# Kernel tuning notes

Hardware: AMD Instinct MI355X
Metric: run time of the kernel (lower is better)

Reference implementation:

```python
import jax, jax.numpy as jnp
import numpy as np

K = 20
NEG_SLOPE = 0.2
BN_EPS = 1e-5


def _knn_idx(x, k):
    # x: (B, N, C) -> indices of k nearest neighbors (B, N, k) (self included)
    sq = jnp.sum(x * x, axis=-1)                      # (B, N)
    d = sq[:, :, None] - 2.0 * jnp.einsum('bnc,bmc->bnm', x, x) + sq[:, None, :]
    return jax.lax.top_k(-d, k)[1]                    # smallest distances


def _bn_lrelu(y, bn):
    g, b, m, v = bn[0], bn[1], bn[2], bn[3]
    y = (y - m) * (g * jax.lax.rsqrt(v + BN_EPS)) + b
    return jnp.where(y > 0, y, NEG_SLOPE * y)


def _edge_conv(x, W, bn, k):
    # x: (B, N, C); W: (O, 2C); returns (B, N, O)
    idx = _knn_idx(x, k)                              # (B, N, k)
    grouped = jnp.take_along_axis(x[:, None, :, :], idx[..., None], axis=2)  # (B, N, k, C)
    center = x[:, :, None, :]
    edge = jnp.concatenate([grouped - center,
                            jnp.broadcast_to(center, grouped.shape)], axis=-1)  # (B, N, k, 2C)
    y = jnp.einsum('bnkc,oc->bnko', edge, W)          # 1x1 conv, no bias
    y = _bn_lrelu(y, bn)
    return jnp.max(y, axis=2)                         # max over neighbors


def setup_inputs() -> dict:
    key = jax.random.key(0)
    ks = jax.random.split(key, 12)
    B, N = 8, 2048
    x = jax.random.normal(ks[0], (B, N, 3), dtype=jnp.float32)

    def w(k_, o, i):
        return jax.random.normal(k_, (o, i), dtype=jnp.float32) * (1.0 / np.sqrt(i))

    def bn(k_, c):
        k1, k2, k3, k4 = jax.random.split(k_, 4)
        gamma = jax.random.uniform(k1, (c,), jnp.float32) + 0.5
        beta = jax.random.normal(k2, (c,), jnp.float32) * 0.1
        mean = jax.random.normal(k3, (c,), jnp.float32) * 0.1
        var = jax.random.uniform(k4, (c,), jnp.float32) + 0.5
        return jnp.stack([gamma, beta, mean, var])    # (4, C)

    return {
        'x': x,
        'W1': w(ks[1], 64, 6),
        'W2': w(ks[2], 64, 128),
        'W3': w(ks[3], 128, 128),
        'W4': w(ks[4], 256, 256),
        'W5': w(ks[5], 1024, 512),
        'bn1': bn(ks[6], 64),
        'bn2': bn(ks[7], 64),
        'bn3': bn(ks[8], 128),
        'bn4': bn(ks[9], 256),
        'bn5': bn(ks[10], 1024),
    }


def reference(x, W1, W2, W3, W4, W5, bn1, bn2, bn3, bn4, bn5):
    x1 = _edge_conv(x, W1, bn1, K)                    # (B, N, 64)
    x2 = _edge_conv(x1, W2, bn2, K)                   # (B, N, 64)
    x3 = _edge_conv(x2, W3, bn3, K)                   # (B, N, 128)
    x4 = _edge_conv(x3, W4, bn4, K)                   # (B, N, 256)
    x_cat = jnp.concatenate([x1, x2, x3, x4], axis=-1)  # (B, N, 512)
    feat = _bn_lrelu(jnp.einsum('bnc,oc->bno', x_cat, W5), bn5)  # (B, N, 1024)
    g_max = jnp.max(feat, axis=1)
    g_avg = jnp.mean(feat, axis=1)
    return jnp.concatenate([g_max, g_avg], axis=-1)   # (B, 2048)
```

## Files before the change

kernel.cpp:

```cpp
#include <hip/hip_runtime.h>
#include <hip/hip_bf16.h>
#include <math.h>

#define KNN 20
constexpr int NPTS = 2048;
constexpr int NBAT = 8;
constexpr int M_TOT = NBAT * NPTS;

__global__ __launch_bounds__(256) void sqnorm_kernel(const float* __restrict__ X, int lda, int C,
                                                     float* __restrict__ sq) {
  int i = blockIdx.x * 256 + threadIdx.x;
  if (i >= M_TOT) return;
  const float* p = X + (size_t)i * lda;
  float s = 0.f;
  for (int c = 0; c < C; ++c) { float v = p[c]; s = fmaf(v, v, s); }
  sq[i] = s;
}

#define INSERT_CAND(key_, j_)                                  \
  if ((key_) < dl[KNN - 1]) {                                  \
    float _k = (key_); int _j = (j_);                          \
    _Pragma("unroll")                                          \
    for (int p = 0; p < KNN; ++p) {                            \
      bool sw = _k < dl[p];                                    \
      float od = dl[p]; int oi = il[p];                        \
      dl[p] = sw ? _k : od; il[p] = sw ? _j : oi;              \
      _k = sw ? od : _k; _j = sw ? oi : _j;                    \
    }                                                          \
  }

template <int C, int CSPLIT>
__global__ __launch_bounds__(256, 8) void knn5_kernel(const float* __restrict__ X, int lda,
                                                      const float* __restrict__ sq,
                                                      float* __restrict__ pd,
                                                      int* __restrict__ pi) {
  constexpr int ROWS = 32, CHK = 64, KB = 32, SEL = 8;
  constexpr int KP = KB + 4;
  constexpr int DP = CHK + 1;
  constexpr int NKB = (C == 3) ? 1 : C / KB;
  constexpr int XI_W = (C == 3) ? 4 : KP;
  constexpr int SMF = ROWS * XI_W + CHK * XI_W + ROWS * DP;
  __shared__ __align__(16) float smem[SMF];
  float* xi = smem;
  float* xj = smem + ROWS * XI_W;
  float* dist = smem + (ROWS + CHK) * XI_W;

  const int b = blockIdx.z;
  const int m0 = blockIdx.x * ROWS;
  const int jsplit = blockIdx.y * (NPTS / CSPLIT);
  const int t = threadIdx.x;
  const int tx = t & 15, ty = t >> 4;
  const int sr = t >> 3, ss = t & 7;
  const float* Xb = X + (size_t)b * NPTS * lda;
  const float* sqb = sq + b * NPTS;

  float dl[KNN]; int il[KNN];
#pragma unroll
  for (int p = 0; p < KNN; ++p) { dl[p] = INFINITY; il[p] = 0x7fffffff; }

  for (int c0 = 0; c0 < NPTS / CSPLIT; c0 += CHK) {
    const int jb = jsplit + c0;
    float acc[2][4] = {};

    if constexpr (C == 3) {
      __syncthreads();
      for (int e = t; e < ROWS * 3; e += 256) {
        int rr = e / 3, cc = e % 3;
        xi[rr * 4 + cc] = Xb[(size_t)(m0 + rr) * lda + cc];
      }
      for (int e = t; e < CHK * 3; e += 256) {
        int rr = e / 3, cc = e % 3;
        xj[rr * 4 + cc] = Xb[(size_t)(jb + rr) * lda + cc];
      }
      __syncthreads();
#pragma unroll
      for (int i = 0; i < 2; ++i) {
        const float* xr = xi + (ty + 16 * i) * 4;
        float x0 = xr[0], x1 = xr[1], x2 = xr[2];
#pragma unroll
        for (int j = 0; j < 4; ++j) {
          const float* xc = xj + (tx + 16 * j) * 4;
          acc[i][j] = fmaf(x0, xc[0], fmaf(x1, xc[1], x2 * xc[2]));
        }
      }
    } else {
#pragma unroll
      for (int kb = 0; kb < NKB; ++kb) {
        __syncthreads();
#pragma unroll
        for (int q = 0; q < 3; ++q) {
          if (q == 0) {
            int rr = t >> 3, cc = t & 7;
            *(float4*)(xi + rr * KP + cc * 4) =
                *(const float4*)(Xb + (size_t)(m0 + rr) * lda + kb * KB + cc * 4);
          } else {
            int f = t + (q - 1) * 256;
            int rr = f >> 3, cc = f & 7;
            *(float4*)(xj + rr * KP + cc * 4) =
                *(const float4*)(Xb + (size_t)(jb + rr) * lda + kb * KB + cc * 4);
          }
        }
        __syncthreads();
#pragma unroll
        for (int k4 = 0; k4 < KB / 4; ++k4) {
          float4 av[2], bv[4];
#pragma unroll
          for (int i = 0; i < 2; ++i) av[i] = *(const float4*)(xi + (ty + 16 * i) * KP + k4 * 4);
#pragma unroll
          for (int j = 0; j < 4; ++j) bv[j] = *(const float4*)(xj + (tx + 16 * j) * KP + k4 * 4);
#pragma unroll
          for (int i = 0; i < 2; ++i)
#pragma unroll
            for (int j = 0; j < 4; ++j) {
              acc[i][j] = fmaf(av[i].x, bv[j].x, acc[i][j]);
              acc[i][j] = fmaf(av[i].y, bv[j].y, acc[i][j]);
              acc[i][j] = fmaf(av[i].z, bv[j].z, acc[i][j]);
              acc[i][j] = fmaf(av[i].w, bv[j].w, acc[i][j]);
            }
        }
      }
    }

    float sqv[4];
#pragma unroll
    for (int j = 0; j < 4; ++j) sqv[j] = sqb[jb + tx + 16 * j];
#pragma unroll
    for (int i = 0; i < 2; ++i) {
      const int row = ty + 16 * i;
      const int sw = (row & 1) << 4;
#pragma unroll
      for (int j = 0; j < 4; ++j)
        dist[row * DP + ((tx + 16 * j) ^ sw)] = fmaf(-2.f, acc[i][j], sqv[j]);
    }
    __syncthreads();

    {
      const int sw = (sr & 1) << 4;
#pragma unroll
      for (int q = 0; q < 8; ++q) {
        float key = dist[sr * DP + ((ss * 8 + q) ^ sw)];
        int jidx = jb + ss * 8 + q;
        INSERT_CAND(key, jidx)
      }
    }
  }

  const size_t base = ((size_t)(b * NPTS + m0 + sr) * CSPLIT + blockIdx.y) * KNN;
  for (int k = 0; k < KNN; ++k) {
    float bd = dl[0]; int bi = il[0];
#pragma unroll
    for (int m = 1; m < SEL; m <<= 1) {
      float od = __shfl_xor(bd, m, SEL);
      int   oi = __shfl_xor(bi, m, SEL);
      if (od < bd || (od == bd && oi < bi)) { bd = od; bi = oi; }
    }
    if (ss == 0) { pd[base + k] = bd; pi[base + k] = bi; }
    const bool pop = (il[0] == bi);
#pragma unroll
    for (int p = 0; p < KNN - 1; ++p) {
      dl[p] = pop ? dl[p + 1] : dl[p];
      il[p] = pop ? il[p + 1] : il[p];
    }
    if (pop) { dl[KNN - 1] = INFINITY; il[KNN - 1] = 0x7fffffff; }
  }
}

template <int NL>
__global__ __launch_bounds__(256) void knnmerge_kernel(const float* __restrict__ pd,
                                                       const int* __restrict__ pi,
                                                       int* __restrict__ knn_out) {
  int row = blockIdx.x * 256 + threadIdx.x;
  if (row >= M_TOT) return;
  const float* d = pd + (size_t)row * NL * KNN;
  const int* ii = pi + (size_t)row * NL * KNN;
  int p[NL];
#pragma unroll
  for (int g = 0; g < NL; ++g) p[g] = 0;
  int* orow = knn_out + (size_t)row * KNN;
  for (int k = 0; k < KNN; ++k) {
    float bd = INFINITY; int bi = 0x7fffffff; int bg = 0;
#pragma unroll
    for (int g = 0; g < NL; ++g) {
      float dd = d[g * KNN + p[g]];
      int iv = ii[g * KNN + p[g]];
      if (dd < bd || (dd == bd && iv < bi)) { bd = dd; bi = iv; bg = g; }
    }
    orow[k] = bi;
#pragma unroll
    for (int g = 0; g < NL; ++g) p[g] += (bg == g) ? 1 : 0;
  }
}

__global__ __launch_bounds__(256) void wcat_kernel(const float* __restrict__ W, int O, int Cc,
                                                   float* __restrict__ out) {
  int i = blockIdx.x * 256 + threadIdx.x;
  if (i >= O * Cc) return;
  int o = i / Cc, c = i % Cc;
  float wd = W[(size_t)o * 2 * Cc + c];
  float wc = W[(size_t)o * 2 * Cc + Cc + c];
  out[(size_t)o * Cc + c] = wd;
  out[(size_t)(O + o) * Cc + c] = wc - wd;
}

template <bool FUSE>
__global__ __launch_bounds__(256) void gemm_kernel(const float* __restrict__ A, int lda, int K,
                                                   const float* __restrict__ Wt, int NO,
                                                   float* __restrict__ out,
                                                   const float* __restrict__ bn) {
  __shared__ float As[16][68];
  __shared__ float Bs[16][68];
  const int t = threadIdx.x;
  const int tx = t & 15, ty = t >> 4;
  const int m0 = blockIdx.x * 64, n0 = blockIdx.y * 64;
  float acc[4][4] = {};

  for (int k0 = 0; k0 < K; k0 += 16) {
#pragma unroll
    for (int q = 0; q < 4; ++q) {
      int e = t + q * 256;
      int rr = e >> 4, cc = e & 15;
      int kk = k0 + cc;
      As[cc][rr] = (kk < K) ? A[(size_t)(m0 + rr) * lda + kk] : 0.f;
      Bs[cc][rr] = (kk < K) ? Wt[(size_t)(n0 + rr) * K + kk] : 0.f;
    }
    __syncthreads();
#pragma unroll
    for (int kk = 0; kk < 16; ++kk) {
      float4 av = *(const float4*)(&As[kk][ty * 4]);
      float4 bv = *(const float4*)(&Bs[kk][tx * 4]);
      float a[4] = {av.x, av.y, av.z, av.w};
      float bb[4] = {bv.x, bv.y, bv.z, bv.w};
#pragma unroll
      for (int i = 0; i < 4; ++i)
#pragma unroll
        for (int j = 0; j < 4; ++j) acc[i][j] = fmaf(a[i], bb[j], acc[i][j]);
    }
    __syncthreads();
  }

#pragma unroll
  for (int i = 0; i < 4; ++i) {
    int row = m0 + ty * 4 + i;
#pragma unroll
    for (int j = 0; j < 4; ++j) {
      int col = n0 + tx * 4 + j;
      float v = acc[i][j];
      if constexpr (FUSE) {
        float g = bn[col], be = bn[NO + col], mm = bn[2 * NO + col], va = bn[3 * NO + col];
        float s = g * rsqrtf(va + 1e-5f);
        v = fmaf(s, v - mm, be);
        v = v > 0.f ? v : 0.2f * v;
      }
      out[(size_t)row * NO + col] = v;
    }
  }
}

__global__ void gathermax_kernel(const float* __restrict__ uv, const int* __restrict__ knn_in,
                                 const float* __restrict__ bn, int O,
                                 float* __restrict__ outc, int ldo) {
  const int n = blockIdx.x;
  const int o = threadIdx.x;
  __shared__ int js[KNN];
  if (o < KNN) js[o] = knn_in[(size_t)n * KNN + o];
  __syncthreads();
  const int b = n >> 11;
  const int ld2 = 2 * O;
  const float* uvb = uv + (size_t)b * NPTS * ld2;
  float m = -INFINITY;
#pragma unroll
  for (int k = 0; k < KNN; ++k) m = fmaxf(m, uvb[(size_t)js[k] * ld2 + o]);
  float u = uv[(size_t)n * ld2 + O + o];
  float g = bn[o], be = bn[O + o], mm = bn[2 * O + o], va = bn[3 * O + o];
  float s = g * rsqrtf(va + 1e-5f);
  float y = fmaf(s, m + u - mm, be);
  y = y > 0.f ? y : 0.2f * y;
  outc[(size_t)n * ldo + o] = y;
}

__global__ __launch_bounds__(256) void reduce1_kernel(const float* __restrict__ feat,
                                                      float* __restrict__ part) {
  const int sp = blockIdx.x;
  const int b = blockIdx.z;
  const int o = blockIdx.y * 256 + threadIdx.x;
  const float* f = feat + ((size_t)b * NPTS + sp * 128) * 1024 + o;
  float mx = -INFINITY, sm = 0.f;
  for (int n = 0; n < 128; ++n) { float v = f[(size_t)n * 1024]; mx = fmaxf(mx, v); sm += v; }
  part[((size_t)(b * 16 + sp)) * 1024 + o] = mx;
  part[131072 + ((size_t)(b * 16 + sp)) * 1024 + o] = sm;
}

__global__ __launch_bounds__(256) void reduce2_kernel(const float* __restrict__ part,
                                                      float* __restrict__ out) {
  const int b = blockIdx.y;
  const int o = blockIdx.x * 256 + threadIdx.x;
  float mx = -INFINITY, sm = 0.f;
  for (int sp = 0; sp < 16; ++sp) {
    mx = fmaxf(mx, part[((size_t)(b * 16 + sp)) * 1024 + o]);
    sm += part[131072 + ((size_t)(b * 16 + sp)) * 1024 + o];
  }
  out[(size_t)b * 2048 + o] = mx;
  out[(size_t)b * 2048 + 1024 + o] = sm * (1.f / 2048.f);
}

extern "C" void kernel_launch(void* const* d_in, const int* in_sizes, int n_in,
                              void* d_out, int out_size, void* d_ws, size_t ws_size,
                              hipStream_t stream) {
  const float* x   = (const float*)d_in[0];
  const float* W1  = (const float*)d_in[1];
  const float* W2  = (const float*)d_in[2];
  const float* W3  = (const float*)d_in[3];
  const float* W4  = (const float*)d_in[4];
  const float* W5  = (const float*)d_in[5];
  const float* bn1 = (const float*)d_in[6];
  const float* bn2 = (const float*)d_in[7];
  const float* bn3 = (const float*)d_in[8];
  const float* bn4 = (const float*)d_in[9];
  const float* bn5 = (const float*)d_in[10];
  float* out = (float*)d_out;

  char* ws = (char*)d_ws;
  float* xcat  = (float*)(ws);
  float* uv    = (float*)(ws + 33554432);
  int*   knnb  = (int*)  (ws + 100663296);
  float* sqb   = (float*)(ws + 101974016);
  float* wcat  = (float*)(ws + 102039552);
  float* part  = (float*)(ws + 102563840);
  float* pd    = uv;
  int*   pi    = (int*)(ws + 33554432 + 22020096);

  const dim3 kg(NPTS / 32, 4, NBAT);

  sqnorm_kernel<<<64, 256, 0, stream>>>(x, 3, 3, sqb);
  knn5_kernel<3, 4><<<kg, 256, 0, stream>>>(x, 3, sqb, pd, pi);
  knnmerge_kernel<4><<<64, 256, 0, stream>>>(pd, pi, knnb);
  wcat_kernel<<<1, 256, 0, stream>>>(W1, 64, 3, wcat);
  gemm_kernel<false><<<dim3(256, 2), 256, 0, stream>>>(x, 3, 3, wcat, 128, uv, nullptr);
  gathermax_kernel<<<16384, 64, 0, stream>>>(uv, knnb, bn1, 64, xcat + 0, 512);

  sqnorm_kernel<<<64, 256, 0, stream>>>(xcat, 512, 64, sqb);
  knn5_kernel<64, 4><<<kg, 256, 0, stream>>>(xcat, 512, sqb, pd, pi);
  knnmerge_kernel<4><<<64, 256, 0, stream>>>(pd, pi, knnb);
  wcat_kernel<<<16, 256, 0, stream>>>(W2, 64, 64, wcat);
  gemm_kernel<false><<<dim3(256, 2), 256, 0, stream>>>(xcat, 512, 64, wcat, 128, uv, nullptr);
  gathermax_kernel<<<16384, 64, 0, stream>>>(uv, knnb, bn2, 64, xcat + 64, 512);

  sqnorm_kernel<<<64, 256, 0, stream>>>(xcat + 64, 512, 64, sqb);
  knn5_kernel<64, 4><<<kg, 256, 0, stream>>>(xcat + 64, 512, sqb, pd, pi);
  knnmerge_kernel<4><<<64, 256, 0, stream>>>(pd, pi, knnb);
  wcat_kernel<<<32, 256, 0, stream>>>(W3, 128, 64, wcat);
  gemm_kernel<false><<<dim3(256, 4), 256, 0, stream>>>(xcat + 64, 512, 64, wcat, 256, uv, nullptr);
  gathermax_kernel<<<16384, 128, 0, stream>>>(uv, knnb, bn3, 128, xcat + 128, 512);

  sqnorm_kernel<<<64, 256, 0, stream>>>(xcat + 128, 512, 128, sqb);
  knn5_kernel<128, 4><<<kg, 256, 0, stream>>>(xcat + 128, 512, sqb, pd, pi);
  knnmerge_kernel<4><<<64, 256, 0, stream>>>(pd, pi, knnb);
  wcat_kernel<<<128, 256, 0, stream>>>(W4, 256, 128, wcat);
  gemm_kernel<false><<<dim3(256, 8), 256, 0, stream>>>(xcat + 128, 512, 128, wcat, 512, uv, nullptr);
  gathermax_kernel<<<16384, 256, 0, stream>>>(uv, knnb, bn4, 256, xcat + 256, 512);

  gemm_kernel<true><<<dim3(256, 16), 256, 0, stream>>>(xcat, 512, 512, W5, 1024, uv, bn5);

  reduce1_kernel<<<dim3(16, 4, 8), 256, 0, stream>>>(uv, part);
  reduce2_kernel<<<dim3(4, 8), 256, 0, stream>>>(part, out);

  (void)in_sizes; (void)n_in; (void)out_size; (void)ws_size;
}
```

Measured before the change: 1.493 ms.

## Drop in-block shuffle merge of kNN lists; merge 32 partial lists in merge kernel

```diff
diff --git a/kernel.cpp b/kernel.cpp
--- a/kernel.cpp
+++ b/kernel.cpp
@@ -30,10 +30,10 @@
   }
 
 template <int C, int CSPLIT>
-__global__ __launch_bounds__(256, 8) void knn5_kernel(const float* __restrict__ X, int lda,
+__global__ __launch_bounds__(256, 8) void knn6_kernel(const float* __restrict__ X, int lda,
                                                       const float* __restrict__ sq,
                                                       float* __restrict__ pd,
-                                                      int* __restrict__ pi) {
+                                                      unsigned short* __restrict__ pi) {
   constexpr int ROWS = 32, CHK = 64, KB = 32, SEL = 8;
   constexpr int KP = KB + 4;
   constexpr int DP = CHK + 1;
@@ -145,34 +145,25 @@
     }
   }
 
-  const size_t base = ((size_t)(b * NPTS + m0 + sr) * CSPLIT + blockIdx.y) * KNN;
-  for (int k = 0; k < KNN; ++k) {
-    float bd = dl[0]; int bi = il[0];
-#pragma unroll
-    for (int m = 1; m < SEL; m <<= 1) {
-      float od = __shfl_xor(bd, m, SEL);
-      int   oi = __shfl_xor(bi, m, SEL);
-      if (od < bd || (od == bd && oi < bi)) { bd = od; bi = oi; }
-    }
-    if (ss == 0) { pd[base + k] = bd; pi[base + k] = bi; }
-    const bool pop = (il[0] == bi);
-#pragma unroll
-    for (int p = 0; p < KNN - 1; ++p) {
-      dl[p] = pop ? dl[p + 1] : dl[p];
-      il[p] = pop ? il[p + 1] : il[p];
-    }
-    if (pop) { dl[KNN - 1] = INFINITY; il[KNN - 1] = 0x7fffffff; }
+  const size_t rowg = (size_t)(b * NPTS + m0 + sr);
+  const int g = blockIdx.y * SEL + ss;
+  float* od = pd + (rowg * (CSPLIT * SEL) + g) * KNN;
+  unsigned short* oi = pi + (rowg * (CSPLIT * SEL) + g) * KNN;
+#pragma unroll
+  for (int p = 0; p < KNN; ++p) {
+    od[p] = dl[p];
+    oi[p] = (unsigned short)(il[p] & 0xFFFF);
   }
 }
 
 template <int NL>
-__global__ __launch_bounds__(256) void knnmerge_kernel(const float* __restrict__ pd,
-                                                       const int* __restrict__ pi,
-                                                       int* __restrict__ knn_out) {
-  int row = blockIdx.x * 256 + threadIdx.x;
+__global__ __launch_bounds__(64) void knnmerge_kernel(const float* __restrict__ pd,
+                                                      const unsigned short* __restrict__ pi,
+                                                      int* __restrict__ knn_out) {
+  int row = blockIdx.x * 64 + threadIdx.x;
   if (row >= M_TOT) return;
   const float* d = pd + (size_t)row * NL * KNN;
-  const int* ii = pi + (size_t)row * NL * KNN;
+  const unsigned short* ii = pi + (size_t)row * NL * KNN;
   int p[NL];
 #pragma unroll
   for (int g = 0; g < NL; ++g) p[g] = 0;
@@ -182,7 +173,7 @@
 #pragma unroll
     for (int g = 0; g < NL; ++g) {
       float dd = d[g * KNN + p[g]];
-      int iv = ii[g * KNN + p[g]];
+      int iv = (int)ii[g * KNN + p[g]];
       if (dd < bd || (dd == bd && iv < bi)) { bd = dd; bi = iv; bg = g; }
     }
     orow[k] = bi;
@@ -326,35 +317,35 @@
   float* sqb   = (float*)(ws + 101974016);
   float* wcat  = (float*)(ws + 102039552);
   float* part  = (float*)(ws + 102563840);
-  float* pd    = uv;
-  int*   pi    = (int*)(ws + 33554432 + 22020096);
+  float*          pd = uv;
+  unsigned short* pi = (unsigned short*)(ws + 33554432 + 41943040);
 
   const dim3 kg(NPTS / 32, 4, NBAT);
 
   sqnorm_kernel<<<64, 256, 0, stream>>>(x, 3, 3, sqb);
-  knn5_kernel<3, 4><<<kg, 256, 0, stream>>>(x, 3, sqb, pd, pi);
-  knnmerge_kernel<4><<<64, 256, 0, stream>>>(pd, pi, knnb);
+  knn6_kernel<3, 4><<<kg, 256, 0, stream>>>(x, 3, sqb, pd, pi);
+  knnmerge_kernel<32><<<256, 64, 0, stream>>>(pd, pi, knnb);
   wcat_kernel<<<1, 256, 0, stream>>>(W1, 64, 3, wcat);
   gemm_kernel<false><<<dim3(256, 2), 256, 0, stream>>>(x, 3, 3, wcat, 128, uv, nullptr);
   gathermax_kernel<<<16384, 64, 0, stream>>>(uv, knnb, bn1, 64, xcat + 0, 512);
 
   sqnorm_kernel<<<64, 256, 0, stream>>>(xcat, 512, 64, sqb);
-  knn5_kernel<64, 4><<<kg, 256, 0, stream>>>(xcat, 512, sqb, pd, pi);
-  knnmerge_kernel<4><<<64, 256, 0, stream>>>(pd, pi, knnb);
+  knn6_kernel<64, 4><<<kg, 256, 0, stream>>>(xcat, 512, sqb, pd, pi);
+  knnmerge_kernel<32><<<256, 64, 0, stream>>>(pd, pi, knnb);
   wcat_kernel<<<16, 256, 0, stream>>>(W2, 64, 64, wcat);
   gemm_kernel<false><<<dim3(256, 2), 256, 0, stream>>>(xcat, 512, 64, wcat, 128, uv, nullptr);
   gathermax_kernel<<<16384, 64, 0, stream>>>(uv, knnb, bn2, 64, xcat + 64, 512);
 
   sqnorm_kernel<<<64, 256, 0, stream>>>(xcat + 64, 512, 64, sqb);
-  knn5_kernel<64, 4><<<kg, 256, 0, stream>>>(xcat + 64, 512, sqb, pd, pi);
-  knnmerge_kernel<4><<<64, 256, 0, stream>>>(pd, pi, knnb);
+  knn6_kernel<64, 4><<<kg, 256, 0, stream>>>(xcat + 64, 512, sqb, pd, pi);
+  knnmerge_kernel<32><<<256, 64, 0, stream>>>(pd, pi, knnb);
   wcat_kernel<<<32, 256, 0, stream>>>(W3, 128, 64, wcat);
   gemm_kernel<false><<<dim3(256, 4), 256, 0, stream>>>(xcat + 64, 512, 64, wcat, 256, uv, nullptr);
   gathermax_kernel<<<16384, 128, 0, stream>>>(uv, knnb, bn3, 128, xcat + 128, 512);
 
   sqnorm_kernel<<<64, 256, 0, stream>>>(xcat + 128, 512, 128, sqb);
-  knn5_kernel<128, 4><<<kg, 256, 0, stream>>>(xcat + 128, 512, sqb, pd, pi);
-  knnmerge_kernel<4><<<64, 256, 0, stream>>>(pd, pi, knnb);
+  knn6_kernel<128, 4><<<kg, 256, 0, stream>>>(xcat + 128, 512, sqb, pd, pi);
+  knnmerge_kernel<32><<<256, 64, 0, stream>>>(pd, pi, knnb);
   wcat_kernel<<<128, 256, 0, stream>>>(W4, 256, 128, wcat);
   gemm_kernel<false><<<dim3(256, 8), 256, 0, stream>>>(xcat + 128, 512, 128, wcat, 512, uv, nullptr);
   gathermax_kernel<<<16384, 256, 0, stream>>>(uv, knnb, bn4, 256, xcat + 256, 512);
```

After: 2.100 ms. +40.7%, slower.
